# Kernel optimization log

Hardware: AMD Instinct MI355X
Metric: run time of the kernel (lower is better)

## Reference

```python
import jax, jax.numpy as jnp
import numpy as np
import math
from jax import lax

B, L = 64, 8192
S = L // 8          # width after 3 stride-(1,2) SAME convs
D = 4 * 5           # height(4) * channels(5) -> per-token feature dim
D_FLAT = S * D


def setup_inputs():
    key = jax.random.key(0)
    ks = jax.random.split(key, 32)
    sc = 0.1
    inp = {
        "inputs": jax.random.randint(ks[0], (B, L), 0, 4, dtype=jnp.int32),
        # conv stack: HWIO kernels, Conv2D(5,(4,4),(1,2),'SAME')
        "conv_w1": sc * jax.random.normal(ks[1], (4, 4, 1, 5), jnp.float32),
        "conv_b1": jnp.zeros((5,), jnp.float32),
        "conv_w2": sc * jax.random.normal(ks[2], (4, 4, 5, 5), jnp.float32),
        "conv_b2": jnp.zeros((5,), jnp.float32),
        "conv_w3": sc * jax.random.normal(ks[3], (4, 4, 5, 5), jnp.float32),
        "conv_b3": jnp.zeros((5,), jnp.float32),
        # 3 SelfAttn blocks, each with K/Q/V projections [D, D]
        "attn1_K": sc * jax.random.normal(ks[4], (D, D), jnp.float32),
        "attn1_Q": sc * jax.random.normal(ks[5], (D, D), jnp.float32),
        "attn1_V": sc * jax.random.normal(ks[6], (D, D), jnp.float32),
        "attn2_K": sc * jax.random.normal(ks[7], (D, D), jnp.float32),
        "attn2_Q": sc * jax.random.normal(ks[8], (D, D), jnp.float32),
        "attn2_V": sc * jax.random.normal(ks[9], (D, D), jnp.float32),
        "attn3_K": sc * jax.random.normal(ks[10], (D, D), jnp.float32),
        "attn3_Q": sc * jax.random.normal(ks[11], (D, D), jnp.float32),
        "attn3_V": sc * jax.random.normal(ks[12], (D, D), jnp.float32),
        # 3 Dense(10) layers (no activation, as in Keras defaults)
        "dense_w1": 0.01 * jax.random.normal(ks[13], (D_FLAT, 10), jnp.float32),
        "dense_b1": jnp.zeros((10,), jnp.float32),
        "dense_w2": sc * jax.random.normal(ks[14], (10, 10), jnp.float32),
        "dense_b2": jnp.zeros((10,), jnp.float32),
        "dense_w3": sc * jax.random.normal(ks[15], (10, 10), jnp.float32),
        "dense_b3": jnp.zeros((10,), jnp.float32),
    }
    return inp


def _conv(x, w, b):
    # NHWC, HWIO, strides (1,2), SAME
    y = lax.conv_general_dilated(x, w, window_strides=(1, 2), padding="SAME",
                                 dimension_numbers=("NHWC", "HWIO", "NHWC"))
    return y + b


def _self_attn(x, Kw, Qw, Vw):
    # x: [B, S, D]; manual causal scaled dot-product attention
    K = x @ Kw
    Q = x @ Qw
    V = x @ Vw
    s = Q.shape[1]
    mask = jnp.triu(jnp.full((s, s), -jnp.inf, dtype=x.dtype), k=1)
    scores = jnp.einsum("bsd,btd->bst", Q, K) / math.sqrt(K.shape[-1]) + mask
    return jax.nn.softmax(scores, axis=-1) @ V


def reference(inputs, conv_w1, conv_b1, conv_w2, conv_b2, conv_w3, conv_b3,
              attn1_K, attn1_Q, attn1_V, attn2_K, attn2_Q, attn2_V,
              attn3_K, attn3_Q, attn3_V,
              dense_w1, dense_b1, dense_w2, dense_b2, dense_w3, dense_b3):
    # one_hot over axis=1 -> [B, 4, L], then channel dim -> [B, 4, L, 1]
    x = jax.nn.one_hot(inputs, 4, axis=1, dtype=jnp.float32)[..., None]
    x = _conv(x, conv_w1, conv_b1)
    x = _conv(x, conv_w2, conv_b2)
    x = _conv(x, conv_w3, conv_b3)            # [B, 4, S, 5]
    # tokens along width, features = height(4) x channels(5)
    x = jnp.transpose(x, (0, 2, 1, 3)).reshape(x.shape[0], S, D)
    x = _self_attn(x, attn1_K, attn1_Q, attn1_V)
    x = _self_attn(x, attn2_K, attn2_Q, attn2_V)
    x = _self_attn(x, attn3_K, attn3_Q, attn3_V)
    x = x.reshape(x.shape[0], -1)             # flatten [B, S*D]
    x = x @ dense_w1 + dense_b1
    x = x @ dense_w2 + dense_b2
    x = x @ dense_w3 + dense_b3               # [B, 10]
    return x
```

## Files before the change

kernel.cpp:

```cpp
#include <hip/hip_runtime.h>
#include <hip/hip_bf16.h>


#define B_ 64
#define L_ 8192
#define S_ 1024
#define D_ 20

typedef unsigned short ushort_t;
typedef __attribute__((ext_vector_type(8))) short short8_t;
typedef __attribute__((ext_vector_type(4))) float f32x4_t;

__device__ __forceinline__ ushort_t f2bf(float f) {
  unsigned u = __float_as_uint(f);
  return (ushort_t)((u + 0x7fffu + ((u >> 16) & 1u)) >> 16);
}
__device__ __forceinline__ float bf2f(ushort_t h) {
  return __uint_as_float(((unsigned)h) << 16);
}

__global__ __launch_bounds__(256) void conv12_kernel(
    const int* __restrict__ inp,
    const float* __restrict__ W1c, const float* __restrict__ B1c,
    const float* __restrict__ W2c, const float* __restrict__ B2c,
    float* __restrict__ out) {
  __shared__ float w1s[80], b1s[5], w2s[400], b2s[5];
  for (int j = threadIdx.x; j < 400; j += 256) w2s[j] = W2c[j];
  if (threadIdx.x < 80)      w1s[threadIdx.x]      = W1c[threadIdx.x];
  else if (threadIdx.x < 85) b1s[threadIdx.x - 80] = B1c[threadIdx.x - 80];
  else if (threadIdx.x < 90) b2s[threadIdx.x - 85] = B2c[threadIdx.x - 85];
  __syncthreads();
  const int idx = blockIdx.x * 256 + threadIdx.x;
  const int b  = idx >> 11;
  const int wo = idx & 2047;
  const int* ib = inp + (size_t)b * L_;
  int iv[10];
#pragma unroll
  for (int t = 0; t < 10; ++t) {
    int g = 4 * wo - 3 + t;
    iv[t] = (g >= 0 && g < L_) ? ib[g] : -100;
  }
  float val[4][4][5];
#pragma unroll
  for (int pos = 0; pos < 4; ++pos) {
    const int w1 = 2 * wo - 1 + pos;
    const bool okp = (w1 >= 0 && w1 < 4096);
#pragma unroll
    for (int hi = 0; hi < 4; ++hi)
#pragma unroll
      for (int ci = 0; ci < 5; ++ci) val[hi][pos][ci] = okp ? b1s[ci] : 0.f;
    if (okp) {
#pragma unroll
      for (int kw = 0; kw < 4; ++kw) {
        const int gw = 2 * w1 - 1 + kw;
        if (gw >= 0 && gw < L_) {
          const int v = iv[2 * pos + kw];
#pragma unroll
          for (int hi = 0; hi < 4; ++hi) {
            const int kh = v - hi + 1;
            if (kh >= 0 && kh < 4) {
#pragma unroll
              for (int ci = 0; ci < 5; ++ci)
                val[hi][pos][ci] += w1s[(kh * 4 + kw) * 5 + ci];
            }
          }
        }
      }
    }
  }
  float acc[4][5];
#pragma unroll
  for (int h = 0; h < 4; ++h)
#pragma unroll
    for (int c = 0; c < 5; ++c) acc[h][c] = b2s[c];
#pragma unroll
  for (int kh = 0; kh < 4; ++kh)
#pragma unroll
    for (int kw = 0; kw < 4; ++kw)
#pragma unroll
      for (int ci = 0; ci < 5; ++ci) {
        const float* wp = w2s + ((kh * 4 + kw) * 5 + ci) * 5;
        float w0 = wp[0], w1v = wp[1], w2v = wp[2], w3 = wp[3], w4 = wp[4];
#pragma unroll
        for (int h = 0; h < 4; ++h) {
          int hi = h - 1 + kh;
          if (hi >= 0 && hi < 4) {
            float x = val[hi][kw][ci];
            acc[h][0] += w0 * x;  acc[h][1] += w1v * x; acc[h][2] += w2v * x;
            acc[h][3] += w3 * x;  acc[h][4] += w4 * x;
          }
        }
      }
  float* ob = out + (size_t)b * 4 * 2048 * 5;
#pragma unroll
  for (int h = 0; h < 4; ++h)
#pragma unroll
    for (int c = 0; c < 5; ++c) ob[(h * 2048 + wo) * 5 + c] = acc[h][c];
}

__global__ __launch_bounds__(256) void conv3_proj_kernel(
    const float* __restrict__ in,
    const float* __restrict__ W,  const float* __restrict__ Bi,
    const float* __restrict__ Kw, const float* __restrict__ Qw,
    const float* __restrict__ Vw,
    ushort_t* __restrict__ Qb, ushort_t* __restrict__ Kb,
    ushort_t* __restrict__ Vt) {
  constexpr int WIN = 2048;
  __shared__ float ws[400], bs[5];
  __shared__ float kw[400], qw[400], vw[400];
  for (int j = threadIdx.x; j < 400; j += 256) {
    ws[j] = W[j]; kw[j] = Kw[j]; qw[j] = Qw[j]; vw[j] = Vw[j];
  }
  if (threadIdx.x < 5) bs[threadIdx.x] = Bi[threadIdx.x];
  __syncthreads();
  const int r  = blockIdx.x * 256 + threadIdx.x;
  const int b  = r >> 10;
  const int wo = r & 1023;
  float val[4][4][5];
#pragma unroll
  for (int hi = 0; hi < 4; ++hi) {
    const float* ir = in + ((size_t)b * 4 + hi) * WIN * 5;
#pragma unroll
    for (int kwp = 0; kwp < 4; ++kwp) {
      int wi = 2 * wo - 1 + kwp;
      bool ok = (wi >= 0 && wi < WIN);
#pragma unroll
      for (int ci = 0; ci < 5; ++ci) val[hi][kwp][ci] = ok ? ir[wi * 5 + ci] : 0.f;
    }
  }
  float acc[4][5];
#pragma unroll
  for (int h = 0; h < 4; ++h)
#pragma unroll
    for (int c = 0; c < 5; ++c) acc[h][c] = bs[c];
#pragma unroll
  for (int kh = 0; kh < 4; ++kh)
#pragma unroll
    for (int kwp = 0; kwp < 4; ++kwp)
#pragma unroll
      for (int ci = 0; ci < 5; ++ci) {
        const float* wp = ws + ((kh * 4 + kwp) * 5 + ci) * 5;
        float w0 = wp[0], w1 = wp[1], w2 = wp[2], w3 = wp[3], w4 = wp[4];
#pragma unroll
        for (int h = 0; h < 4; ++h) {
          int hi = h - 1 + kh;
          if (hi >= 0 && hi < 4) {
            float x = val[hi][kwp][ci];
            acc[h][0] += w0 * x; acc[h][1] += w1 * x; acc[h][2] += w2 * x;
            acc[h][3] += w3 * x; acc[h][4] += w4 * x;
          }
        }
      }
  float x[D_];
#pragma unroll
  for (int h = 0; h < 4; ++h)
#pragma unroll
    for (int c = 0; c < 5; ++c) x[h * 5 + c] = acc[h][c];
  float q[D_], k[D_], v[D_];
#pragma unroll
  for (int j = 0; j < D_; ++j) { q[j] = 0.f; k[j] = 0.f; v[j] = 0.f; }
#pragma unroll
  for (int i = 0; i < D_; ++i) {
#pragma unroll
    for (int j = 0; j < D_; ++j) {
      q[j] += x[i] * qw[i * D_ + j];
      k[j] += x[i] * kw[i * D_ + j];
      v[j] += x[i] * vw[i * D_ + j];
    }
  }
  const float sc = 0.22360679774997896f;
  ushort_t qt[32], kt[32];
#pragma unroll
  for (int j = 0; j < D_; ++j) { qt[j] = f2bf(q[j] * sc); kt[j] = f2bf(k[j]); }
#pragma unroll
  for (int j = D_; j < 32; ++j) { qt[j] = 0; kt[j] = 0; }
  int4* qd = (int4*)(Qb + (size_t)r * 32);
  int4* kd = (int4*)(Kb + (size_t)r * 32);
#pragma unroll
  for (int j = 0; j < 4; ++j) {
    qd[j] = *(const int4*)(qt + 8 * j);
    kd[j] = *(const int4*)(kt + 8 * j);
  }
  ushort_t* vbase = Vt + ((size_t)b * 32) * 1024 + wo;
#pragma unroll
  for (int d = 0; d < D_; ++d) vbase[d * 1024] = f2bf(v[d]);
}

__global__ __launch_bounds__(256) void proj_kernel(
    const float* __restrict__ X,
    const float* __restrict__ Kw, const float* __restrict__ Qw,
    const float* __restrict__ Vw,
    ushort_t* __restrict__ Qb, ushort_t* __restrict__ Kb,
    ushort_t* __restrict__ Vt) {
  __shared__ float kw[400], qw[400], vw[400];
  for (int j = threadIdx.x; j < 400; j += 256) {
    kw[j] = Kw[j]; qw[j] = Qw[j]; vw[j] = Vw[j];
  }
  __syncthreads();
  int r = blockIdx.x * 256 + threadIdx.x;
  const float4* xr4 = (const float4*)(X + (size_t)r * D_);
  float x[D_];
#pragma unroll
  for (int i = 0; i < 5; ++i) {
    float4 t = xr4[i];
    x[4*i] = t.x; x[4*i+1] = t.y; x[4*i+2] = t.z; x[4*i+3] = t.w;
  }
  float q[D_], k[D_], v[D_];
#pragma unroll
  for (int j = 0; j < D_; ++j) { q[j] = 0.f; k[j] = 0.f; v[j] = 0.f; }
#pragma unroll
  for (int i = 0; i < D_; ++i) {
#pragma unroll
    for (int j = 0; j < D_; ++j) {
      q[j] += x[i] * qw[i * D_ + j];
      k[j] += x[i] * kw[i * D_ + j];
      v[j] += x[i] * vw[i * D_ + j];
    }
  }
  const float sc = 0.22360679774997896f;
  ushort_t qt[32], kt[32];
#pragma unroll
  for (int j = 0; j < D_; ++j) { qt[j] = f2bf(q[j] * sc); kt[j] = f2bf(k[j]); }
#pragma unroll
  for (int j = D_; j < 32; ++j) { qt[j] = 0; kt[j] = 0; }
  int4* qd = (int4*)(Qb + (size_t)r * 32);
  int4* kd = (int4*)(Kb + (size_t)r * 32);
#pragma unroll
  for (int j = 0; j < 4; ++j) {
    qd[j] = *(const int4*)(qt + 8 * j);
    kd[j] = *(const int4*)(kt + 8 * j);
  }
  const int bb = r >> 10, ss = r & 1023;
  ushort_t* vbase = Vt + ((size_t)bb * 32) * 1024 + ss;
#pragma unroll
  for (int d = 0; d < D_; ++d) vbase[d * 1024] = f2bf(v[d]);
}

#define TT_ 128
__global__ __launch_bounds__(256) void attn_kernel(
    const ushort_t* __restrict__ Qb, const ushort_t* __restrict__ Kb,
    const ushort_t* __restrict__ Vt, float* __restrict__ out) {
  const int b     = blockIdx.y;
  const int strip = (blockIdx.x + 4 * (blockIdx.y >> 4)) & 15;
  const int q0    = strip * 64;
  const int tid   = threadIdx.x;
  const int w     = tid >> 6;
  const int lane  = tid & 63;
  const int n     = lane & 15;
  const int quad  = lane >> 4;
  const int qbase = q0 + 16 * w;
  __shared__ ushort_t kts[128 * 40];
  __shared__ ushort_t vts[32 * 136];
  __shared__ ushort_t pts[4][16 * 40];
  const ushort_t* KbB = Kb + (size_t)b * 1024 * 32;
  const ushort_t* VtB = Vt + (size_t)b * 32 * 1024;
  short8_t qfrag = *(const short8_t*)(Qb + ((size_t)(b * 1024 + qbase + n)) * 32 + quad * 8);
  f32x4_t oA = {0.f, 0.f, 0.f, 0.f};
  f32x4_t oB = {0.f, 0.f, 0.f, 0.f};
  f32x4_t lac = {0.f, 0.f, 0.f, 0.f};
  const f32x4_t zero = {0.f, 0.f, 0.f, 0.f};
  const int Tw = qbase + 16;
  const int nt = q0 + 64;
  ushort_t* prow = pts[w];
  for (int t0 = 0; t0 < nt; t0 += TT_) {
    __syncthreads();
    for (int i = tid; i < 512; i += 256) {
      int row = i >> 2, qc = i & 3;
      *(int4*)(kts + row * 40 + qc * 8) =
          *(const int4*)(KbB + (size_t)(t0 + row) * 32 + qc * 8);
    }
    for (int i = tid; i < 320; i += 256) {
      int row = i >> 4, cc = i & 15;
      *(int4*)(vts + row * 136 + cc * 8) =
          *(const int4*)(VtB + (size_t)row * 1024 + t0 + cc * 8);
    }
    __syncthreads();
#pragma unroll 1
    for (int cc = 0; cc < 4; ++cc) {
      const int tc = t0 + cc * 32;
      if (tc >= Tw) break;
      const short8_t kfA = *(const short8_t*)(kts + (cc * 32 + n) * 40 + quad * 8);
      const short8_t kfB = *(const short8_t*)(kts + (cc * 32 + 16 + n) * 40 + quad * 8);
      f32x4_t sA = __builtin_amdgcn_mfma_f32_16x16x32_bf16(qfrag, kfA, zero, 0, 0, 0);
      f32x4_t sB = __builtin_amdgcn_mfma_f32_16x16x32_bf16(qfrag, kfB, zero, 0, 0, 0);
#pragma unroll
      for (int r = 0; r < 4; ++r) {
        const int qg = qbase + quad * 4 + r;
        float pA = (tc + n      <= qg) ? __expf(sA[r]) : 0.f;
        float pB = (tc + 16 + n <= qg) ? __expf(sB[r]) : 0.f;
        ushort_t hA = f2bf(pA), hB = f2bf(pB);
        lac[r] += bf2f(hA) + bf2f(hB);
        prow[(quad * 4 + r) * 40 + n]      = hA;
        prow[(quad * 4 + r) * 40 + 16 + n] = hB;
      }
      __asm__ volatile("s_waitcnt lgkmcnt(0)" ::: "memory");
      short8_t pfrag = *(const short8_t*)(prow + n * 40 + quad * 8);
      const short8_t vfA = *(const short8_t*)(vts + n * 136 + cc * 32 + quad * 8);
      const short8_t vfB = *(const short8_t*)(vts + (16 + n) * 136 + cc * 32 + quad * 8);
      oA = __builtin_amdgcn_mfma_f32_16x16x32_bf16(pfrag, vfA, oA, 0, 0, 0);
      oB = __builtin_amdgcn_mfma_f32_16x16x32_bf16(pfrag, vfB, oB, 0, 0, 0);
    }
  }
#pragma unroll
  for (int m = 1; m <= 8; m <<= 1) {
#pragma unroll
    for (int r = 0; r < 4; ++r) lac[r] += __shfl_xor(lac[r], m, 64);
  }
  float* ob = out + ((size_t)(b * 1024 + qbase)) * 20;
#pragma unroll
  for (int r = 0; r < 4; ++r) {
    const float inv = 1.f / lac[r];
    const int qq = quad * 4 + r;
    ob[qq * 20 + n] = oA[r] * inv;
    if (n < 4) ob[qq * 20 + 16 + n] = oB[r] * inv;
  }
}

__global__ __launch_bounds__(256) void transpose_w1(
    const float* __restrict__ W1,
    float* __restrict__ W1T) {
  int idx = blockIdx.x * 256 + threadIdx.x;
  int j = idx / 20480;
  int i = idx % 20480;
  W1T[idx] = W1[i * 10 + j];
}

__global__ __launch_bounds__(256) void dense1_partial(
    const float* __restrict__ X,
    const float* __restrict__ W1T,
    float* __restrict__ part) {
  const int b = blockIdx.x;
  const int s = blockIdx.y;
  const float4* xb = (const float4*)(X + (size_t)b * 20480 + s * 5120);
  float acc[10];
#pragma unroll
  for (int j = 0; j < 10; ++j) acc[j] = 0.f;
  for (int i = threadIdx.x; i < 1280; i += 256) {
    float4 xv = xb[i];
#pragma unroll
    for (int j = 0; j < 10; ++j) {
      float4 wv = ((const float4*)(W1T + (size_t)j * 20480 + s * 5120))[i];
      acc[j] += xv.x * wv.x + xv.y * wv.y + xv.z * wv.z + xv.w * wv.w;
    }
  }
  __shared__ float red[256][10];
#pragma unroll
  for (int j = 0; j < 10; ++j) red[threadIdx.x][j] = acc[j];
  __syncthreads();
  for (int off = 128; off > 0; off >>= 1) {
    if (threadIdx.x < (unsigned)off) {
#pragma unroll
      for (int j = 0; j < 10; ++j) red[threadIdx.x][j] += red[threadIdx.x + off][j];
    }
    __syncthreads();
  }
  if (threadIdx.x < 10) part[(b * 4 + s) * 10 + threadIdx.x] = red[0][threadIdx.x];
}

__global__ __launch_bounds__(64) void dense_final(
    const float* __restrict__ part,
    const float* __restrict__ B1,
    const float* __restrict__ W2, const float* __restrict__ B2,
    const float* __restrict__ W3, const float* __restrict__ B3,
    float* __restrict__ out) {
  const int b = blockIdx.x;
  __shared__ float y1[10], y2[10];
  if (threadIdx.x < 10) {
    int j = threadIdx.x;
    y1[j] = part[(b*4+0)*10 + j] + part[(b*4+1)*10 + j] +
            part[(b*4+2)*10 + j] + part[(b*4+3)*10 + j] + B1[j];
  }
  __syncthreads();
  if (threadIdx.x < 10) {
    int j = threadIdx.x;
    float s = B2[j];
#pragma unroll
    for (int i = 0; i < 10; ++i) s += y1[i] * W2[i * 10 + j];
    y2[j] = s;
  }
  __syncthreads();
  if (threadIdx.x < 10) {
    int j = threadIdx.x;
    float s = B3[j];
#pragma unroll
    for (int i = 0; i < 10; ++i) s += y2[i] * W3[i * 10 + j];
    out[b * 10 + j] = s;
  }
}

extern "C" void kernel_launch(void* const* d_in, const int* in_sizes, int n_in,
                              void* d_out, int out_size, void* d_ws, size_t ws_size,
                              hipStream_t stream) {
  const int*   inp = (const int*)d_in[0];
  const float* cw1 = (const float*)d_in[1];
  const float* cb1 = (const float*)d_in[2];
  const float* cw2 = (const float*)d_in[3];
  const float* cb2 = (const float*)d_in[4];
  const float* cw3 = (const float*)d_in[5];
  const float* cb3 = (const float*)d_in[6];
  const float* a1K = (const float*)d_in[7];
  const float* a1Q = (const float*)d_in[8];
  const float* a1V = (const float*)d_in[9];
  const float* a2K = (const float*)d_in[10];
  const float* a2Q = (const float*)d_in[11];
  const float* a2V = (const float*)d_in[12];
  const float* a3K = (const float*)d_in[13];
  const float* a3Q = (const float*)d_in[14];
  const float* a3V = (const float*)d_in[15];
  const float* dw1 = (const float*)d_in[16];
  const float* db1 = (const float*)d_in[17];
  const float* dw2 = (const float*)d_in[18];
  const float* db2 = (const float*)d_in[19];
  const float* dw3 = (const float*)d_in[20];
  const float* db3 = (const float*)d_in[21];
  float* outp = (float*)d_out;

  float* wsf = (float*)d_ws;
  float*    c2   = wsf + 5242880;
  float*    x    = wsf + 7864320;
  ushort_t* qb   = (ushort_t*)(wsf);
  ushort_t* kb   = (ushort_t*)(wsf + 1048576);
  ushort_t* vt   = (ushort_t*)(wsf + 2097152);
  float*    o    = wsf + 3145728;
  float*    part = wsf + 4456448;
  float*    w1t  = wsf + 4459008;

  conv12_kernel<<<512, 256, 0, stream>>>(inp, cw1, cb1, cw2, cb2, c2);
  transpose_w1<<<800, 256, 0, stream>>>(dw1, w1t);

  conv3_proj_kernel<<<256, 256, 0, stream>>>(c2, cw3, cb3, a1K, a1Q, a1V, qb, kb, vt);
  attn_kernel<<<dim3(16, 64), 256, 0, stream>>>(qb, kb, vt, o);

  proj_kernel<<<256, 256, 0, stream>>>(o, a2K, a2Q, a2V, qb, kb, vt);
  attn_kernel<<<dim3(16, 64), 256, 0, stream>>>(qb, kb, vt, x);

  proj_kernel<<<256, 256, 0, stream>>>(x, a3K, a3Q, a3V, qb, kb, vt);
  attn_kernel<<<dim3(16, 64), 256, 0, stream>>>(qb, kb, vt, o);

  dense1_partial<<<dim3(64, 4), 256, 0, stream>>>(o, w1t, part);
  dense_final<<<64, 64, 0, stream>>>(part, db1, dw2, db2, dw3, db3, outp);
}
```

Before: 244.4 us.

## Fuse next-layer QKV projection into attention kernel epilogue with ping-pong buffers

Removes the two standalone projection kernels and computes the next attention block's Q/K/V projection inside the attention kernel's epilogue. Each wave stages its normalized output rows in shared memory, and four lanes per row each compute a slice of the projection. The bf16 Q/K/Vt buffers are double-buffered because other blocks may still read the current ones. This saves two launches and the fp32 round trip of the intermediate activations, at the cost of extra shared memory (about 10KB), scattered 2-byte global stores, and weight loading in every attention block.

```diff
diff --git a/kernel.cpp b/kernel.cpp
--- a/kernel.cpp
+++ b/kernel.cpp
@@ -186,60 +186,15 @@
   for (int d = 0; d < D_; ++d) vbase[d * 1024] = f2bf(v[d]);
 }
 
-__global__ __launch_bounds__(256) void proj_kernel(
-    const float* __restrict__ X,
-    const float* __restrict__ Kw, const float* __restrict__ Qw,
-    const float* __restrict__ Vw,
-    ushort_t* __restrict__ Qb, ushort_t* __restrict__ Kb,
-    ushort_t* __restrict__ Vt) {
-  __shared__ float kw[400], qw[400], vw[400];
-  for (int j = threadIdx.x; j < 400; j += 256) {
-    kw[j] = Kw[j]; qw[j] = Qw[j]; vw[j] = Vw[j];
-  }
-  __syncthreads();
-  int r = blockIdx.x * 256 + threadIdx.x;
-  const float4* xr4 = (const float4*)(X + (size_t)r * D_);
-  float x[D_];
-#pragma unroll
-  for (int i = 0; i < 5; ++i) {
-    float4 t = xr4[i];
-    x[4*i] = t.x; x[4*i+1] = t.y; x[4*i+2] = t.z; x[4*i+3] = t.w;
-  }
-  float q[D_], k[D_], v[D_];
-#pragma unroll
-  for (int j = 0; j < D_; ++j) { q[j] = 0.f; k[j] = 0.f; v[j] = 0.f; }
-#pragma unroll
-  for (int i = 0; i < D_; ++i) {
-#pragma unroll
-    for (int j = 0; j < D_; ++j) {
-      q[j] += x[i] * qw[i * D_ + j];
-      k[j] += x[i] * kw[i * D_ + j];
-      v[j] += x[i] * vw[i * D_ + j];
-    }
-  }
-  const float sc = 0.22360679774997896f;
-  ushort_t qt[32], kt[32];
-#pragma unroll
-  for (int j = 0; j < D_; ++j) { qt[j] = f2bf(q[j] * sc); kt[j] = f2bf(k[j]); }
-#pragma unroll
-  for (int j = D_; j < 32; ++j) { qt[j] = 0; kt[j] = 0; }
-  int4* qd = (int4*)(Qb + (size_t)r * 32);
-  int4* kd = (int4*)(Kb + (size_t)r * 32);
-#pragma unroll
-  for (int j = 0; j < 4; ++j) {
-    qd[j] = *(const int4*)(qt + 8 * j);
-    kd[j] = *(const int4*)(kt + 8 * j);
-  }
-  const int bb = r >> 10, ss = r & 1023;
-  ushort_t* vbase = Vt + ((size_t)bb * 32) * 1024 + ss;
-#pragma unroll
-  for (int d = 0; d < D_; ++d) vbase[d * 1024] = f2bf(v[d]);
-}
-
 #define TT_ 128
+template <bool FUSE>
 __global__ __launch_bounds__(256) void attn_kernel(
     const ushort_t* __restrict__ Qb, const ushort_t* __restrict__ Kb,
-    const ushort_t* __restrict__ Vt, float* __restrict__ out) {
+    const ushort_t* __restrict__ Vt, float* __restrict__ out,
+    const float* __restrict__ Kw2, const float* __restrict__ Qw2,
+    const float* __restrict__ Vw2,
+    ushort_t* __restrict__ Qb2, ushort_t* __restrict__ Kb2,
+    ushort_t* __restrict__ Vt2) {
   const int b     = blockIdx.y;
   const int strip = (blockIdx.x + 4 * (blockIdx.y >> 4)) & 15;
   const int q0    = strip * 64;
@@ -252,6 +207,24 @@
   __shared__ ushort_t kts[128 * 40];
   __shared__ ushort_t vts[32 * 136];
   __shared__ ushort_t pts[4][16 * 40];
+  __shared__ float    pw[1200];
+  __shared__ float    ox[4][320];
+  if (FUSE) {
+    float tmp[5];
+#pragma unroll
+    for (int u = 0; u < 5; ++u) {
+      int j = tid + u * 256;
+      if (j < 1200) {
+        int m = j / 400, oo = j - m * 400;
+        tmp[u] = (m == 0) ? Kw2[oo] : (m == 1) ? Qw2[oo] : Vw2[oo];
+      }
+    }
+#pragma unroll
+    for (int u = 0; u < 5; ++u) {
+      int j = tid + u * 256;
+      if (j < 1200) pw[j] = tmp[u];
+    }
+  }
   const ushort_t* KbB = Kb + (size_t)b * 1024 * 32;
   const ushort_t* VtB = Vt + (size_t)b * 32 * 1024;
   short8_t qfrag = *(const short8_t*)(Qb + ((size_t)(b * 1024 + qbase + n)) * 32 + quad * 8);
@@ -306,13 +279,63 @@
 #pragma unroll
     for (int r = 0; r < 4; ++r) lac[r] += __shfl_xor(lac[r], m, 64);
   }
-  float* ob = out + ((size_t)(b * 1024 + qbase)) * 20;
-#pragma unroll
-  for (int r = 0; r < 4; ++r) {
-    const float inv = 1.f / lac[r];
-    const int qq = quad * 4 + r;
-    ob[qq * 20 + n] = oA[r] * inv;
-    if (n < 4) ob[qq * 20 + 16 + n] = oB[r] * inv;
+  if (!FUSE) {
+    float* ob = out + ((size_t)(b * 1024 + qbase)) * 20;
+#pragma unroll
+    for (int r = 0; r < 4; ++r) {
+      const float inv = 1.f / lac[r];
+      const int qq = quad * 4 + r;
+      ob[qq * 20 + n] = oA[r] * inv;
+      if (n < 4) ob[qq * 20 + 16 + n] = oB[r] * inv;
+    }
+  } else {
+    float* oxw = ox[w];
+#pragma unroll
+    for (int r = 0; r < 4; ++r) {
+      const float inv = 1.f / lac[r];
+      const int qq = quad * 4 + r;
+      oxw[qq * 20 + n] = oA[r] * inv;
+      if (n < 4) oxw[qq * 20 + 16 + n] = oB[r] * inv;
+    }
+    __asm__ volatile("s_waitcnt lgkmcnt(0)" ::: "memory");
+    const int row  = lane >> 2;
+    const int part = lane & 3;
+    float x[D_];
+#pragma unroll
+    for (int i = 0; i < D_; ++i) x[i] = oxw[row * 20 + i];
+    float qv[5], kv[5], vv[5];
+#pragma unroll
+    for (int jj = 0; jj < 5; ++jj) { qv[jj] = 0.f; kv[jj] = 0.f; vv[jj] = 0.f; }
+#pragma unroll
+    for (int i = 0; i < D_; ++i) {
+      const float xi = x[i];
+#pragma unroll
+      for (int jj = 0; jj < 5; ++jj) {
+        const int j = 5 * part + jj;
+        kv[jj] += xi * pw[i * 20 + j];
+        qv[jj] += xi * pw[400 + i * 20 + j];
+        vv[jj] += xi * pw[800 + i * 20 + j];
+      }
+    }
+    const float sc = 0.22360679774997896f;
+    const int rg = b * 1024 + qbase + row;
+    const int s  = rg & 1023;
+#pragma unroll
+    for (int jj = 0; jj < 5; ++jj) {
+      const int j = 5 * part + jj;
+      Kb2[(size_t)rg * 32 + j] = f2bf(kv[jj]);
+      Qb2[(size_t)rg * 32 + j] = f2bf(qv[jj] * sc);
+      Vt2[(size_t)b * 32768 + (size_t)j * 1024 + s] = f2bf(vv[jj]);
+    }
+    if (part == 0) {
+#pragma unroll
+      for (int u = 0; u < 6; ++u)
+        *(unsigned*)(Kb2 + (size_t)rg * 32 + 20 + 2 * u) = 0u;
+    } else if (part == 1) {
+#pragma unroll
+      for (int u = 0; u < 6; ++u)
+        *(unsigned*)(Qb2 + (size_t)rg * 32 + 20 + 2 * u) = 0u;
+    }
   }
 }
 
@@ -416,26 +439,27 @@
   float* outp = (float*)d_out;
 
   float* wsf = (float*)d_ws;
-  float*    c2   = wsf + 5242880;
-  float*    x    = wsf + 7864320;
-  ushort_t* qb   = (ushort_t*)(wsf);
-  ushort_t* kb   = (ushort_t*)(wsf + 1048576);
-  ushort_t* vt   = (ushort_t*)(wsf + 2097152);
+  ushort_t* qbA  = (ushort_t*)(wsf);
+  ushort_t* kbA  = (ushort_t*)(wsf + 1048576);
+  ushort_t* vtA  = (ushort_t*)(wsf + 2097152);
   float*    o    = wsf + 3145728;
   float*    part = wsf + 4456448;
   float*    w1t  = wsf + 4459008;
+  ushort_t* qbB  = (ushort_t*)(wsf + 4663808);
+  ushort_t* kbB  = (ushort_t*)(wsf + 5712384);
+  ushort_t* vtB  = (ushort_t*)(wsf + 6760960);
+  float*    c2   = wsf + 5242880;
 
   conv12_kernel<<<512, 256, 0, stream>>>(inp, cw1, cb1, cw2, cb2, c2);
   transpose_w1<<<800, 256, 0, stream>>>(dw1, w1t);
 
-  conv3_proj_kernel<<<256, 256, 0, stream>>>(c2, cw3, cb3, a1K, a1Q, a1V, qb, kb, vt);
-  attn_kernel<<<dim3(16, 64), 256, 0, stream>>>(qb, kb, vt, o);
-
-  proj_kernel<<<256, 256, 0, stream>>>(o, a2K, a2Q, a2V, qb, kb, vt);
-  attn_kernel<<<dim3(16, 64), 256, 0, stream>>>(qb, kb, vt, x);
-
-  proj_kernel<<<256, 256, 0, stream>>>(x, a3K, a3Q, a3V, qb, kb, vt);
-  attn_kernel<<<dim3(16, 64), 256, 0, stream>>>(qb, kb, vt, o);
+  conv3_proj_kernel<<<256, 256, 0, stream>>>(c2, cw3, cb3, a1K, a1Q, a1V, qbA, kbA, vtA);
+  attn_kernel<true><<<dim3(16, 64), 256, 0, stream>>>(
+      qbA, kbA, vtA, nullptr, a2K, a2Q, a2V, qbB, kbB, vtB);
+  attn_kernel<true><<<dim3(16, 64), 256, 0, stream>>>(
+      qbB, kbB, vtB, nullptr, a3K, a3Q, a3V, qbA, kbA, vtA);
+  attn_kernel<false><<<dim3(16, 64), 256, 0, stream>>>(
+      qbA, kbA, vtA, o, nullptr, nullptr, nullptr, nullptr, nullptr, nullptr);
 
   dense1_partial<<<dim3(64, 4), 256, 0, stream>>>(o, w1t, part);
   dense_final<<<64, 64, 0, stream>>>(part, db1, dw2, db2, dw3, db3, outp);
```

After: 245.2 us. No clear change (+0.3%).
